# Kernel optimization log

Hardware: AMD Instinct MI355X
Metric: run time of the kernel (lower is better)

The kernel has to match this reference:

```python
import jax, jax.numpy as jnp
import numpy as np

NEG_SLOPE = 0.2  # PyG GATConv default negative_slope
EPS = 1e-16


def gat_conv(x, W, att_src, att_dst, bias, src, dst, heads, out_ch, concat):
    """PyG-style GATConv (eval mode, self-loops already included in src/dst).
    x: [N, F_in]; W: [heads*out_ch, F_in]; att_src/att_dst: [1, heads, out_ch]; bias: [heads*out_ch] or [out_ch].
    """
    N = x.shape[0]
    h = (x @ W.T).reshape(N, heads, out_ch)            # [N, H, C]
    a_src = (h * att_src).sum(-1)                      # [N, H]
    a_dst = (h * att_dst).sum(-1)                      # [N, H]
    alpha = jax.nn.leaky_relu(a_src[src] + a_dst[dst], NEG_SLOPE)  # [E, H]
    # segment softmax over destination nodes
    amax = jax.ops.segment_max(alpha, dst, num_segments=N)         # [N, H]
    ex = jnp.exp(alpha - amax[dst])
    denom = jax.ops.segment_sum(ex, dst, num_segments=N)           # [N, H]
    coef = ex / (denom[dst] + EPS)                                 # [E, H]
    out = jax.ops.segment_sum(h[src] * coef[:, :, None], dst, num_segments=N)  # [N, H, C]
    if concat:
        out = out.reshape(N, heads * out_ch)
    else:
        out = out.mean(axis=1)
    return out + bias


def setup_inputs() -> dict:
    key = jax.random.key(0)
    ks = jax.random.split(key, 10)
    N, F_in, H, C, OUT, E = 50000, 128, 4, 64, 2, 800000
    x = jax.random.normal(ks[0], (N, F_in), dtype=jnp.float32)
    edge_index = jax.random.randint(ks[1], (2, E), 0, N, dtype=jnp.int64)
    glorot = lambda k, shp: jax.random.normal(k, shp, dtype=jnp.float32) * jnp.sqrt(2.0 / (shp[0] + shp[-1]))
    W1 = glorot(ks[2], (H * C, F_in))
    att_src1 = glorot(ks[3], (1, H, C))
    att_dst1 = glorot(ks[4], (1, H, C))
    b1 = jnp.zeros((H * C,), dtype=jnp.float32)
    W2 = glorot(ks[5], (1 * OUT, H * C))
    att_src2 = glorot(ks[6], (1, 1, OUT))
    att_dst2 = glorot(ks[7], (1, 1, OUT))
    b2 = jnp.zeros((OUT,), dtype=jnp.float32)
    return {"x": x, "edge_index": edge_index, "W1": W1, "att_src1": att_src1,
            "att_dst1": att_dst1, "b1": b1, "W2": W2, "att_src2": att_src2,
            "att_dst2": att_dst2, "b2": b2}


def reference(x, edge_index, W1, att_src1, att_dst1, b1, W2, att_src2, att_dst2, b2):
    N = x.shape[0]
    loop = jnp.arange(N, dtype=edge_index.dtype)
    src = jnp.concatenate([edge_index[0], loop])   # add self-loops (PyG default)
    dst = jnp.concatenate([edge_index[1], loop])
    h = gat_conv(x, W1, att_src1, att_dst1, b1, src, dst, heads=4, out_ch=64, concat=True)
    h = jax.nn.relu(h)
    out = gat_conv(h, W2, att_src2, att_dst2, b2, src, dst, heads=1, out_ch=2, concat=False)
    return out
```

## Files before the change

### kernel.cpp

```cpp
#include <hip/hip_runtime.h>
#include <hip/hip_bf16.h>
#include <stdint.h>
#include <math.h>

#define NEG_SLOPE 0.2f
#define EPSV 1e-16f
#define SLOT 64
#define NBQ 128
#define NBUCKET 391
#define CAPA 32
#define EPB 8192
#define OVCAP 64
#define NW1C 16

#define KA 0.8656170245333781f
#define KB 0.5770780163555854f

typedef __attribute__((ext_vector_type(8))) short bf16x8;
typedef __attribute__((ext_vector_type(4))) float f32x4;

static __device__ __forceinline__ float b2f(unsigned short u) {
    union { float f; uint32_t i; } v; v.i = ((uint32_t)u) << 16; return v.f;
}
static __device__ __forceinline__ uint32_t qpk(float a, float b) {
    union { float f; uint32_t u; } x, y; x.f = a; y.f = b;
    return ((x.u + 0x8000u) >> 16) | ((y.u + 0x8000u) & 0xFFFF0000u);
}

__global__ __launch_bounds__(256) void prep_bin_kernel(
    const int* __restrict__ ei, int E,
    const float* __restrict__ W1,
    const float* __restrict__ b1, const float* __restrict__ W2,
    unsigned int* __restrict__ bins, unsigned short* __restrict__ counts,
    unsigned int* __restrict__ gov, unsigned int* __restrict__ govcnt,
    unsigned short* __restrict__ w1p,
    float* __restrict__ b1p, float* __restrict__ w2p0, float* __restrict__ w2p1,
    unsigned short* __restrict__ h1, float4* __restrict__ a_src1v,
    float4* __restrict__ h2pk,
    int N, int nblk_binA)
{
    const int b = blockIdx.x, t = threadIdx.x;

    if (b < nblk_binA) {
        __shared__ unsigned int binS[NBUCKET * CAPA];
        __shared__ unsigned int binC[NBUCKET];
        __shared__ unsigned int ovn;
        const int blk = b;

        for (int i = t; i < NBUCKET; i += 256) binC[i] = 0;
        if (t == 0) ovn = 0;
        __syncthreads();

        const int e_base = blk * EPB;
        for (int i = 0; i < EPB / 256; ++i) {
            int e = e_base + i * 256 + t;
            if (e < E) {
                int s = ei[e], d = ei[E + e];
                int bk = d >> 7;
                unsigned int w = (unsigned int)s | ((unsigned int)(d & 127) << 16)
                               | ((unsigned int)bk << 23);
                unsigned int r = atomicAdd(&binC[bk], 1u);
                if (r < CAPA) binS[bk * CAPA + r] = w;
                else {
                    unsigned int o = atomicAdd(&ovn, 1u);
                    if (o < OVCAP) gov[blk * OVCAP + o] = w;
                }
            }
        }
        __syncthreads();

        for (int wdx = t; wdx < NBUCKET * CAPA; wdx += 256) {
            int bk = wdx >> 5, sl = wdx & 31;
            bins[((size_t)bk * nblk_binA + blk) * CAPA + sl] = binS[wdx];
        }
        for (int i = t; i < NBUCKET; i += 256) {
            unsigned int c = binC[i];
            counts[(size_t)i * nblk_binA + blk] = (unsigned short)(c < CAPA ? c : CAPA);
        }
        if (t == 0) govcnt[blk] = (ovn < OVCAP ? ovn : OVCAP);
    } else if (b < nblk_binA + NW1C) {
        int idx = (b - nblk_binA) * 256 + t;
        int c = idx >> 4, oct = idx & 15;
        int ct = c >> 4, l15 = c & 15;
        int kk = oct >> 2, quad = oct & 3;
        const float* sp = W1 + (size_t)c * 128 + oct * 8;
        float4 u0 = *(const float4*)(sp);
        float4 u1 = *(const float4*)(sp + 4);
        uint4 w;
        w.x = qpk(u0.x, u0.y); w.y = qpk(u0.z, u0.w);
        w.z = qpk(u1.x, u1.y); w.w = qpk(u1.z, u1.w);
        *(uint4*)(w1p + (size_t)(((kk * 16 + ct) * 4 + quad) * 128 + l15 * 8)) = w;
    } else {
        int cp = t;
        int c = (cp & 15) * 16 + (cp >> 4);
        b1p[cp]  = b1[c];
        w2p0[cp] = W2[c];
        w2p1[cp] = W2[256 + c];
        if (t < 32)
            ((uint4*)(h1 + (size_t)N * 256))[t] = make_uint4(0, 0, 0, 0);
        else if (t == 32)
            a_src1v[N] = make_float4(-1e4f, -1e4f, -1e4f, -1e4f);
        else if (t == 33)
            h2pk[N] = make_float4(0.f, 0.f, -1e4f, 0.f);
    }
}

__global__ __launch_bounds__(256, 3) void gemm_front_kernel(
    const float* __restrict__ x,
    const unsigned short* __restrict__ w1p,
    const float* __restrict__ att_src1, const float* __restrict__ att_dst1,
    unsigned short* __restrict__ h1,
    float4* __restrict__ a_src1v, float4* __restrict__ a_dst1v,
    int N)
{
    const int t = threadIdx.x;
    const int wv = t >> 6, lane = t & 63;
    const int l15 = lane & 15, quad = lane >> 4;
    const int m0 = blockIdx.x * 64 + wv * 16;

    union { bf16x8 v; uint32_t u[4]; } A[4];
    {
        int m = m0 + l15;
        int mr = m < N ? m : N - 1;
        const float* ap = x + (size_t)mr * 128 + quad * 8;
        #pragma unroll
        for (int kk = 0; kk < 4; ++kk) {
            float4 u0 = *(const float4*)(ap + kk * 32);
            float4 u1 = *(const float4*)(ap + kk * 32 + 4);
            A[kk].u[0] = qpk(u0.x, u0.y);
            A[kk].u[1] = qpk(u0.z, u0.w);
            A[kk].u[2] = qpk(u1.x, u1.y);
            A[kk].u[3] = qpk(u1.z, u1.w);
        }
    }

    f32x4 acc[16];
    #pragma unroll
    for (int ct = 0; ct < 16; ++ct) acc[ct] = (f32x4){0.f, 0.f, 0.f, 0.f};

    const size_t bbase = (size_t)quad * 128 + l15 * 8;
    #pragma unroll
    for (int kk = 0; kk < 4; ++kk) {
        #pragma unroll
        for (int ct = 0; ct < 16; ++ct) {
            bf16x8 Bv = *(const bf16x8*)(w1p + (size_t)(kk * 16 + ct) * 512 + bbase);
            acc[ct] = __builtin_amdgcn_mfma_f32_16x16x32_bf16(A[kk].v, Bv, acc[ct], 0, 0, 0);
        }
    }

    #pragma unroll
    for (int r = 0; r < 4; ++r) {
        int m = m0 + quad * 4 + r;
        if (m < N) {
            uint32_t u[8];
            #pragma unroll
            for (int j = 0; j < 8; ++j)
                u[j] = qpk(acc[2 * j][r], acc[2 * j + 1][r]);
            uint4* hp = (uint4*)(h1 + (size_t)m * 256 + l15 * 16);
            hp[0] = make_uint4(u[0], u[1], u[2], u[3]);
            hp[1] = make_uint4(u[4], u[5], u[6], u[7]);
        }
    }

    float as_l[16], ad_l[16];
    #pragma unroll
    for (int ct = 0; ct < 16; ++ct) {
        as_l[ct] = att_src1[ct * 16 + l15];
        ad_l[ct] = att_dst1[ct * 16 + l15];
    }
    #pragma unroll
    for (int r = 0; r < 4; ++r) {
        float ps[4] = {0.f, 0.f, 0.f, 0.f};
        float pd[4] = {0.f, 0.f, 0.f, 0.f};
        #pragma unroll
        for (int ct = 0; ct < 16; ++ct) {
            ps[ct >> 2] += acc[ct][r] * as_l[ct];
            pd[ct >> 2] += acc[ct][r] * ad_l[ct];
        }
        #pragma unroll
        for (int off = 1; off < 16; off <<= 1) {
            #pragma unroll
            for (int hh = 0; hh < 4; ++hh) {
                ps[hh] += __shfl_xor(ps[hh], off);
                pd[hh] += __shfl_xor(pd[hh], off);
            }
        }
        int m = m0 + quad * 4 + r;
        if (l15 == 0 && m < N) {
            a_src1v[m] = make_float4(ps[0], ps[1], ps[2], ps[3]);
            a_dst1v[m] = make_float4(pd[0], pd[1], pd[2], pd[3]);
        }
    }
}

__global__ __launch_bounds__(256) void csr_build_kernel(
    const unsigned int* __restrict__ bins, const unsigned short* __restrict__ counts,
    const unsigned int* __restrict__ gov, const unsigned int* __restrict__ govcnt,
    int* __restrict__ deg, unsigned short* __restrict__ csr16,
    int N, int nblk_binA)
{
    const int b = blockIdx.x, t = threadIdx.x;
    const int base = b * NBQ;
    __shared__ unsigned short lcsr[NBQ * SLOT];
    __shared__ unsigned int ldeg[NBQ];

    const unsigned int pad2 = ((unsigned int)N << 16) | (unsigned int)N;
    unsigned int* lc32 = (unsigned int*)lcsr;
    for (int i = t; i < NBQ * SLOT / 2; i += 256) lc32[i] = pad2;
    __syncthreads();
    for (int i = t; i < NBQ; i += 256) {
        ldeg[i] = 1;
        lcsr[i << 6] = (unsigned short)(base + i);
    }
    __syncthreads();

    if (t < 2 * nblk_binA) {
        int cell = t >> 1;
        int c = counts[(size_t)b * nblk_binA + cell];
        const unsigned int* cp = bins + ((size_t)b * nblk_binA + cell) * CAPA;
        for (int r = (t & 1); r < c; r += 2) {
            unsigned int w = cp[r];
            int dl = (w >> 16) & 127;
            unsigned int rank = atomicAdd(&ldeg[dl], 1u);
            if (rank < SLOT) lcsr[(dl << 6) + rank] = (unsigned short)(w & 0xFFFF);
        }
    }
    for (int idx = t; idx < nblk_binA * OVCAP; idx += 256) {
        int blk = idx >> 6, sl = idx & (OVCAP - 1);
        if (sl < (int)govcnt[blk]) {
            unsigned int w = gov[idx];
            if ((int)(w >> 23) == b) {
                int dl = (w >> 16) & 127;
                unsigned int rank = atomicAdd(&ldeg[dl], 1u);
                if (rank < SLOT) lcsr[(dl << 6) + rank] = (unsigned short)(w & 0xFFFF);
            }
        }
    }
    __syncthreads();

    const int nn = min(NBQ, N - base);
    uint4* dst = (uint4*)(csr16 + (size_t)base * SLOT);
    const uint4* src = (const uint4*)lcsr;
    for (int i = t; i < nn * 8; i += 256) dst[i] = src[i];
    for (int i = t; i < nn; i += 256) deg[base + i] = (int)ldeg[i];
}

__global__ __launch_bounds__(256) void agg1_layer2_kernel(
    const int* __restrict__ deg, const unsigned short* __restrict__ csr16,
    const float* __restrict__ a_src1, const float* __restrict__ a_dst1,
    const unsigned short* __restrict__ h1,
    const float* __restrict__ b1p,
    const float* __restrict__ w2p0, const float* __restrict__ w2p1,
    const float* __restrict__ as2, const float* __restrict__ ad2,
    float4* __restrict__ h2pk, int N)
{
    const int wv = threadIdx.x >> 6, lane = threadIdx.x & 63;
    const int half = lane >> 5, ll = lane & 31;
    const int n = blockIdx.x * 4 + wv;
    if (n >= N) return;
    const int h0 = (ll & 1) * 2;
    const unsigned short* cs = csr16 + (size_t)n * SLOT;
    const int dn = min(deg[n], 57);
    const float2 adh = *(const float2*)(a_dst1 + (size_t)n * 4 + h0);

    const int iters  = (dn + 1) >> 1;
    const int iters4 = (iters + 3) & ~3;

    const unsigned llo = (unsigned)ll * 16u;
    const unsigned ho  = (unsigned)h0 * 4u;
    const char* h1b = (const char*)h1;
    const char* asb = (const char*)a_src1;

    float acc[8] = {0.f, 0.f, 0.f, 0.f, 0.f, 0.f, 0.f, 0.f};
    float den0 = 0.f, den1 = 0.f;

    auto consume = [&](float2 av, uint4 r) {
        float a0 = av.x + adh.x, a1 = av.y + adh.y;
        float e0 = exp2f(fmaf(KB, fabsf(a0), KA * a0));
        float e1 = exp2f(fmaf(KB, fabsf(a1), KA * a1));
        den0 += e0; den1 += e1;
        union { unsigned u; float f; } lo, hi;
        lo.u = r.x << 16; hi.u = r.x & 0xFFFF0000u;
        acc[0] = fmaf(e0, lo.f, acc[0]); acc[1] = fmaf(e0, hi.f, acc[1]);
        lo.u = r.y << 16; hi.u = r.y & 0xFFFF0000u;
        acc[2] = fmaf(e0, lo.f, acc[2]); acc[3] = fmaf(e0, hi.f, acc[3]);
        lo.u = r.z << 16; hi.u = r.z & 0xFFFF0000u;
        acc[4] = fmaf(e1, lo.f, acc[4]); acc[5] = fmaf(e1, hi.f, acc[5]);
        lo.u = r.w << 16; hi.u = r.w & 0xFFFF0000u;
        acc[6] = fmaf(e1, lo.f, acc[6]); acc[7] = fmaf(e1, hi.f, acc[7]);
    };

    int ia = half, ib = half + 2, ic = half + 4, id = half + 6;
    unsigned s0 = cs[ia], s1 = cs[ib], s2 = cs[ic], s3 = cs[id];
    uint4  rA = *(const uint4*)(h1b + s0 * 512u + llo);
    float2 aA = *(const float2*)(asb + s0 * 16u + ho);
    uint4  rB = *(const uint4*)(h1b + s1 * 512u + llo);
    float2 aB = *(const float2*)(asb + s1 * 16u + ho);
    uint4  rC = *(const uint4*)(h1b + s2 * 512u + llo);
    float2 aC = *(const float2*)(asb + s2 * 16u + ho);
    uint4  rD = *(const uint4*)(h1b + s3 * 512u + llo);
    float2 aD = *(const float2*)(asb + s3 * 16u + ho);

    for (int k = 0; k + 4 < iters4; k += 4) {
        unsigned n0 = cs[ia + 8], n1 = cs[ib + 8], n2 = cs[ic + 8], n3 = cs[id + 8];
        consume(aA, rA);
        rA = *(const uint4*)(h1b + n0 * 512u + llo);
        aA = *(const float2*)(asb + n0 * 16u + ho);
        consume(aB, rB);
        rB = *(const uint4*)(h1b + n1 * 512u + llo);
        aB = *(const float2*)(asb + n1 * 16u + ho);
        consume(aC, rC);
        rC = *(const uint4*)(h1b + n2 * 512u + llo);
        aC = *(const float2*)(asb + n2 * 16u + ho);
        consume(aD, rD);
        rD = *(const uint4*)(h1b + n3 * 512u + llo);
        aD = *(const float2*)(asb + n3 * 16u + ho);
        ia += 8; ib += 8; ic += 8; id += 8;
    }
    consume(aA, rA); consume(aB, rB); consume(aC, rC); consume(aD, rD);

    #pragma unroll
    for (int k = 0; k < 8; ++k) acc[k] += __shfl_xor(acc[k], 32);
    den0 += __shfl_xor(den0, 32);
    den1 += __shfl_xor(den1, 32);

    const float inv0 = 1.f / (den0 + EPSV);
    const float inv1 = 1.f / (den1 + EPSV);
    const int c0 = ll * 8;
    float4 ba = *(const float4*)(b1p + c0);
    float4 bb = *(const float4*)(b1p + c0 + 4);
    float v[8];
    v[0] = acc[0] * inv0 + ba.x; v[1] = acc[1] * inv0 + ba.y;
    v[2] = acc[2] * inv0 + ba.z; v[3] = acc[3] * inv0 + ba.w;
    v[4] = acc[4] * inv1 + bb.x; v[5] = acc[5] * inv1 + bb.y;
    v[6] = acc[6] * inv1 + bb.z; v[7] = acc[7] * inv1 + bb.w;
    #pragma unroll
    for (int k = 0; k < 8; ++k) v[k] = v[k] > 0.f ? v[k] : 0.f;

    float4 w0a = *(const float4*)(w2p0 + c0);
    float4 w0b = *(const float4*)(w2p0 + c0 + 4);
    float4 w1a = *(const float4*)(w2p1 + c0);
    float4 w1b = *(const float4*)(w2p1 + c0 + 4);
    float p0 = v[0]*w0a.x + v[1]*w0a.y + v[2]*w0a.z + v[3]*w0a.w
             + v[4]*w0b.x + v[5]*w0b.y + v[6]*w0b.z + v[7]*w0b.w;
    float p1 = v[0]*w1a.x + v[1]*w1a.y + v[2]*w1a.z + v[3]*w1a.w
             + v[4]*w1b.x + v[5]*w1b.y + v[6]*w1b.z + v[7]*w1b.w;
    #pragma unroll
    for (int off = 16; off; off >>= 1) {
        p0 += __shfl_xor(p0, off);
        p1 += __shfl_xor(p1, off);
    }
    if (lane == 0) {
        h2pk[n] = make_float4(p0, p1,
                              p0 * as2[0] + p1 * as2[1],
                              p0 * ad2[0] + p1 * ad2[1]);
    }
}

__global__ __launch_bounds__(256) void aggregate2_csr_kernel(
    const int* __restrict__ deg, const unsigned short* __restrict__ csr16,
    const float4* __restrict__ h2pk,
    const float* __restrict__ b2, float* __restrict__ out, int N)
{
    const int wv = threadIdx.x >> 6, lane = threadIdx.x & 63;
    const int g = lane >> 4, q = lane & 15;
    const int n = blockIdx.x * 16 + wv * 4 + g;
    if (n >= N) return;
    const unsigned short* cs = csr16 + (size_t)n * SLOT;
    const int dn = min(deg[n], SLOT);
    float ad = h2pk[n].w;
    float den = 0.f, num0 = 0.f, num1 = 0.f;
    const char* hb = (const char*)h2pk;
    const int trip = (dn + 15) >> 4;
    for (int k = 0; k < trip; ++k) {
        unsigned s = cs[q + (k << 4)];
        float4 hq = *(const float4*)(hb + s * 16u);
        float aa = hq.z + ad;
        float ex = exp2f(fmaf(KB, fabsf(aa), KA * aa));
        den += ex;
        num0 = fmaf(ex, hq.x, num0);
        num1 = fmaf(ex, hq.y, num1);
    }
    #pragma unroll
    for (int off = 8; off; off >>= 1) {
        den  += __shfl_xor(den, off);
        num0 += __shfl_xor(num0, off);
        num1 += __shfl_xor(num1, off);
    }
    if (q == 0) {
        float inv = 1.f / (den + EPSV);
        out[(size_t)n * 2]     = num0 * inv + b2[0];
        out[(size_t)n * 2 + 1] = num1 * inv + b2[1];
    }
}

extern "C" void kernel_launch(void* const* d_in, const int* in_sizes, int n_in,
                              void* d_out, int out_size, void* d_ws, size_t ws_size,
                              hipStream_t stream)
{
    const float* x   = (const float*)d_in[0];
    const int*   ei  = (const int*)d_in[1];
    const float* W1  = (const float*)d_in[2];
    const float* as1 = (const float*)d_in[3];
    const float* ad1 = (const float*)d_in[4];
    const float* b1  = (const float*)d_in[5];
    const float* W2  = (const float*)d_in[6];
    const float* as2 = (const float*)d_in[7];
    const float* ad2 = (const float*)d_in[8];
    const float* b2p = (const float*)d_in[9];

    const int N  = in_sizes[0] / 128;
    const int E  = in_sizes[1] / 2;

    const int NB        = (N + NBQ - 1) / NBQ;
    const int nblk_binA = (E + EPB - 1) / EPB;

    char* ws = (char*)d_ws;
    size_t off = 0;
    auto alloc = [&](size_t bytes) -> char* {
        char* p = ws + off;
        off = (off + bytes + 255) & ~(size_t)255;
        return p;
    };
    unsigned short* h1 = (unsigned short*)alloc((size_t)(N + 1) * 256 * 2);
    float* a_src1  = (float*)alloc((size_t)(N + 1) * 4 * 4);
    float* a_dst1  = (float*)alloc((size_t)N * 4 * 4);
    float4* h2pk   = (float4*)alloc((size_t)(N + 1) * 16);
    float* b1pp    = (float*)alloc((size_t)256 * 4);
    float* w2p0    = (float*)alloc((size_t)256 * 4);
    float* w2p1    = (float*)alloc((size_t)256 * 4);
    int*   deg     = (int*)alloc((size_t)N * 4);
    unsigned short* csr16 = (unsigned short*)alloc((size_t)N * SLOT * 2);
    unsigned int*   bins  = (unsigned int*)alloc((size_t)NB * nblk_binA * CAPA * 4);
    unsigned short* cnts  = (unsigned short*)alloc((size_t)NB * nblk_binA * 2);
    unsigned int*   gov   = (unsigned int*)alloc((size_t)nblk_binA * OVCAP * 4);
    unsigned int*   govcnt= (unsigned int*)alloc((size_t)nblk_binA * 4);
    unsigned short* w1pb  = (unsigned short*)alloc((size_t)256 * 128 * 2);

    prep_bin_kernel<<<nblk_binA + NW1C + 1, 256, 0, stream>>>(
        ei, E, W1, b1, W2,
        bins, cnts, gov, govcnt, w1pb, b1pp, w2p0, w2p1,
        h1, (float4*)a_src1, h2pk, N, nblk_binA);
    gemm_front_kernel<<<(N + 63) / 64, 256, 0, stream>>>(
        x, w1pb, as1, ad1, h1, (float4*)a_src1, (float4*)a_dst1, N);
    csr_build_kernel<<<NB, 256, 0, stream>>>(
        bins, cnts, gov, govcnt, deg, csr16, N, nblk_binA);
    agg1_layer2_kernel<<<(N + 3) / 4, 256, 0, stream>>>(
        deg, csr16, a_src1, a_dst1, h1,
        b1pp, w2p0, w2p1, as2, ad2, h2pk, N);
    aggregate2_csr_kernel<<<(N + 15) / 16, 256, 0, stream>>>(
        deg, csr16, h2pk, b2p, (float*)d_out, N);
}
```

Measured before the change: 201.0 us.

## Merge GEMM and CSR build into one launch; trim padded aggregation iterations

Combines the layer-1 GEMM kernel and the CSR build kernel into a single launch whose blocks branch by block index, so the two independent stages can run concurrently and one kernel launch is saved. The aggregation kernel no longer rounds its loop count up to a multiple of four; it consumes only the prefetched edges that remain, which skips wasted padded gathers. The merged kernel makes GEMM blocks carry the 16KB shared buffer used only by CSR blocks and shares a launch-bound setting across both paths, which may lower occupancy for the GEMM part.

```diff
diff --git a/kernel.cpp b/kernel.cpp
--- a/kernel.cpp
+++ b/kernel.cpp
@@ -105,144 +105,143 @@
     }
 }
 
-__global__ __launch_bounds__(256, 3) void gemm_front_kernel(
+__global__ __launch_bounds__(256, 3) void gemm_csr_kernel(
     const float* __restrict__ x,
     const unsigned short* __restrict__ w1p,
     const float* __restrict__ att_src1, const float* __restrict__ att_dst1,
     unsigned short* __restrict__ h1,
     float4* __restrict__ a_src1v, float4* __restrict__ a_dst1v,
-    int N)
-{
-    const int t = threadIdx.x;
-    const int wv = t >> 6, lane = t & 63;
-    const int l15 = lane & 15, quad = lane >> 4;
-    const int m0 = blockIdx.x * 64 + wv * 16;
-
-    union { bf16x8 v; uint32_t u[4]; } A[4];
-    {
-        int m = m0 + l15;
-        int mr = m < N ? m : N - 1;
-        const float* ap = x + (size_t)mr * 128 + quad * 8;
-        #pragma unroll
-        for (int kk = 0; kk < 4; ++kk) {
-            float4 u0 = *(const float4*)(ap + kk * 32);
-            float4 u1 = *(const float4*)(ap + kk * 32 + 4);
-            A[kk].u[0] = qpk(u0.x, u0.y);
-            A[kk].u[1] = qpk(u0.z, u0.w);
-            A[kk].u[2] = qpk(u1.x, u1.y);
-            A[kk].u[3] = qpk(u1.z, u1.w);
-        }
-    }
-
-    f32x4 acc[16];
-    #pragma unroll
-    for (int ct = 0; ct < 16; ++ct) acc[ct] = (f32x4){0.f, 0.f, 0.f, 0.f};
-
-    const size_t bbase = (size_t)quad * 128 + l15 * 8;
-    #pragma unroll
-    for (int kk = 0; kk < 4; ++kk) {
-        #pragma unroll
-        for (int ct = 0; ct < 16; ++ct) {
-            bf16x8 Bv = *(const bf16x8*)(w1p + (size_t)(kk * 16 + ct) * 512 + bbase);
-            acc[ct] = __builtin_amdgcn_mfma_f32_16x16x32_bf16(A[kk].v, Bv, acc[ct], 0, 0, 0);
-        }
-    }
-
-    #pragma unroll
-    for (int r = 0; r < 4; ++r) {
-        int m = m0 + quad * 4 + r;
-        if (m < N) {
-            uint32_t u[8];
-            #pragma unroll
-            for (int j = 0; j < 8; ++j)
-                u[j] = qpk(acc[2 * j][r], acc[2 * j + 1][r]);
-            uint4* hp = (uint4*)(h1 + (size_t)m * 256 + l15 * 16);
-            hp[0] = make_uint4(u[0], u[1], u[2], u[3]);
-            hp[1] = make_uint4(u[4], u[5], u[6], u[7]);
-        }
-    }
-
-    float as_l[16], ad_l[16];
-    #pragma unroll
-    for (int ct = 0; ct < 16; ++ct) {
-        as_l[ct] = att_src1[ct * 16 + l15];
-        ad_l[ct] = att_dst1[ct * 16 + l15];
-    }
-    #pragma unroll
-    for (int r = 0; r < 4; ++r) {
-        float ps[4] = {0.f, 0.f, 0.f, 0.f};
-        float pd[4] = {0.f, 0.f, 0.f, 0.f};
-        #pragma unroll
-        for (int ct = 0; ct < 16; ++ct) {
-            ps[ct >> 2] += acc[ct][r] * as_l[ct];
-            pd[ct >> 2] += acc[ct][r] * ad_l[ct];
-        }
-        #pragma unroll
-        for (int off = 1; off < 16; off <<= 1) {
-            #pragma unroll
-            for (int hh = 0; hh < 4; ++hh) {
-                ps[hh] += __shfl_xor(ps[hh], off);
-                pd[hh] += __shfl_xor(pd[hh], off);
-            }
-        }
-        int m = m0 + quad * 4 + r;
-        if (l15 == 0 && m < N) {
-            a_src1v[m] = make_float4(ps[0], ps[1], ps[2], ps[3]);
-            a_dst1v[m] = make_float4(pd[0], pd[1], pd[2], pd[3]);
-        }
-    }
-}
-
-__global__ __launch_bounds__(256) void csr_build_kernel(
     const unsigned int* __restrict__ bins, const unsigned short* __restrict__ counts,
     const unsigned int* __restrict__ gov, const unsigned int* __restrict__ govcnt,
     int* __restrict__ deg, unsigned short* __restrict__ csr16,
-    int N, int nblk_binA)
+    int N, int nblk_gemm, int nblk_binA)
 {
-    const int b = blockIdx.x, t = threadIdx.x;
-    const int base = b * NBQ;
+    const int t = threadIdx.x;
     __shared__ unsigned short lcsr[NBQ * SLOT];
     __shared__ unsigned int ldeg[NBQ];
 
-    const unsigned int pad2 = ((unsigned int)N << 16) | (unsigned int)N;
-    unsigned int* lc32 = (unsigned int*)lcsr;
-    for (int i = t; i < NBQ * SLOT / 2; i += 256) lc32[i] = pad2;
-    __syncthreads();
-    for (int i = t; i < NBQ; i += 256) {
-        ldeg[i] = 1;
-        lcsr[i << 6] = (unsigned short)(base + i);
-    }
-    __syncthreads();
-
-    if (t < 2 * nblk_binA) {
-        int cell = t >> 1;
-        int c = counts[(size_t)b * nblk_binA + cell];
-        const unsigned int* cp = bins + ((size_t)b * nblk_binA + cell) * CAPA;
-        for (int r = (t & 1); r < c; r += 2) {
-            unsigned int w = cp[r];
-            int dl = (w >> 16) & 127;
-            unsigned int rank = atomicAdd(&ldeg[dl], 1u);
-            if (rank < SLOT) lcsr[(dl << 6) + rank] = (unsigned short)(w & 0xFFFF);
-        }
-    }
-    for (int idx = t; idx < nblk_binA * OVCAP; idx += 256) {
-        int blk = idx >> 6, sl = idx & (OVCAP - 1);
-        if (sl < (int)govcnt[blk]) {
-            unsigned int w = gov[idx];
-            if ((int)(w >> 23) == b) {
+    if (blockIdx.x < nblk_gemm) {
+        const int wv = t >> 6, lane = t & 63;
+        const int l15 = lane & 15, quad = lane >> 4;
+        const int m0 = blockIdx.x * 64 + wv * 16;
+
+        union { bf16x8 v; uint32_t u[4]; } A[4];
+        {
+            int m = m0 + l15;
+            int mr = m < N ? m : N - 1;
+            const float* ap = x + (size_t)mr * 128 + quad * 8;
+            #pragma unroll
+            for (int kk = 0; kk < 4; ++kk) {
+                float4 u0 = *(const float4*)(ap + kk * 32);
+                float4 u1 = *(const float4*)(ap + kk * 32 + 4);
+                A[kk].u[0] = qpk(u0.x, u0.y);
+                A[kk].u[1] = qpk(u0.z, u0.w);
+                A[kk].u[2] = qpk(u1.x, u1.y);
+                A[kk].u[3] = qpk(u1.z, u1.w);
+            }
+        }
+
+        f32x4 acc[16];
+        #pragma unroll
+        for (int ct = 0; ct < 16; ++ct) acc[ct] = (f32x4){0.f, 0.f, 0.f, 0.f};
+
+        const size_t bbase = (size_t)quad * 128 + l15 * 8;
+        #pragma unroll
+        for (int kk = 0; kk < 4; ++kk) {
+            #pragma unroll
+            for (int ct = 0; ct < 16; ++ct) {
+                bf16x8 Bv = *(const bf16x8*)(w1p + (size_t)(kk * 16 + ct) * 512 + bbase);
+                acc[ct] = __builtin_amdgcn_mfma_f32_16x16x32_bf16(A[kk].v, Bv, acc[ct], 0, 0, 0);
+            }
+        }
+
+        #pragma unroll
+        for (int r = 0; r < 4; ++r) {
+            int m = m0 + quad * 4 + r;
+            if (m < N) {
+                uint32_t u[8];
+                #pragma unroll
+                for (int j = 0; j < 8; ++j)
+                    u[j] = qpk(acc[2 * j][r], acc[2 * j + 1][r]);
+                uint4* hp = (uint4*)(h1 + (size_t)m * 256 + l15 * 16);
+                hp[0] = make_uint4(u[0], u[1], u[2], u[3]);
+                hp[1] = make_uint4(u[4], u[5], u[6], u[7]);
+            }
+        }
+
+        float as_l[16], ad_l[16];
+        #pragma unroll
+        for (int ct = 0; ct < 16; ++ct) {
+            as_l[ct] = att_src1[ct * 16 + l15];
+            ad_l[ct] = att_dst1[ct * 16 + l15];
+        }
+        #pragma unroll
+        for (int r = 0; r < 4; ++r) {
+            float ps[4] = {0.f, 0.f, 0.f, 0.f};
+            float pd[4] = {0.f, 0.f, 0.f, 0.f};
+            #pragma unroll
+            for (int ct = 0; ct < 16; ++ct) {
+                ps[ct >> 2] += acc[ct][r] * as_l[ct];
+                pd[ct >> 2] += acc[ct][r] * ad_l[ct];
+            }
+            #pragma unroll
+            for (int off = 1; off < 16; off <<= 1) {
+                #pragma unroll
+                for (int hh = 0; hh < 4; ++hh) {
+                    ps[hh] += __shfl_xor(ps[hh], off);
+                    pd[hh] += __shfl_xor(pd[hh], off);
+                }
+            }
+            int m = m0 + quad * 4 + r;
+            if (l15 == 0 && m < N) {
+                a_src1v[m] = make_float4(ps[0], ps[1], ps[2], ps[3]);
+                a_dst1v[m] = make_float4(pd[0], pd[1], pd[2], pd[3]);
+            }
+        }
+    } else {
+        const int b = blockIdx.x - nblk_gemm;
+        const int base = b * NBQ;
+
+        const unsigned int pad2 = ((unsigned int)N << 16) | (unsigned int)N;
+        unsigned int* lc32 = (unsigned int*)lcsr;
+        for (int i = t; i < NBQ * SLOT / 2; i += 256) lc32[i] = pad2;
+        __syncthreads();
+        for (int i = t; i < NBQ; i += 256) {
+            ldeg[i] = 1;
+            lcsr[i << 6] = (unsigned short)(base + i);
+        }
+        __syncthreads();
+
+        if (t < 2 * nblk_binA) {
+            int cell = t >> 1;
+            int c = counts[(size_t)b * nblk_binA + cell];
+            const unsigned int* cp = bins + ((size_t)b * nblk_binA + cell) * CAPA;
+            for (int r = (t & 1); r < c; r += 2) {
+                unsigned int w = cp[r];
                 int dl = (w >> 16) & 127;
                 unsigned int rank = atomicAdd(&ldeg[dl], 1u);
                 if (rank < SLOT) lcsr[(dl << 6) + rank] = (unsigned short)(w & 0xFFFF);
             }
         }
-    }
-    __syncthreads();
-
-    const int nn = min(NBQ, N - base);
-    uint4* dst = (uint4*)(csr16 + (size_t)base * SLOT);
-    const uint4* src = (const uint4*)lcsr;
-    for (int i = t; i < nn * 8; i += 256) dst[i] = src[i];
-    for (int i = t; i < nn; i += 256) deg[base + i] = (int)ldeg[i];
+        for (int idx = t; idx < nblk_binA * OVCAP; idx += 256) {
+            int blk = idx >> 6, sl = idx & (OVCAP - 1);
+            if (sl < (int)govcnt[blk]) {
+                unsigned int w = gov[idx];
+                if ((int)(w >> 23) == b) {
+                    int dl = (w >> 16) & 127;
+                    unsigned int rank = atomicAdd(&ldeg[dl], 1u);
+                    if (rank < SLOT) lcsr[(dl << 6) + rank] = (unsigned short)(w & 0xFFFF);
+                }
+            }
+        }
+        __syncthreads();
+
+        const int nn = min(NBQ, N - base);
+        uint4* dst = (uint4*)(csr16 + (size_t)base * SLOT);
+        const uint4* src = (const uint4*)lcsr;
+        for (int i = t; i < nn * 8; i += 256) dst[i] = src[i];
+        for (int i = t; i < nn; i += 256) deg[base + i] = (int)ldeg[i];
+    }
 }
 
 __global__ __launch_bounds__(256) void agg1_layer2_kernel(
@@ -263,8 +262,7 @@
     const int dn = min(deg[n], 57);
     const float2 adh = *(const float2*)(a_dst1 + (size_t)n * 4 + h0);
 
-    const int iters  = (dn + 1) >> 1;
-    const int iters4 = (iters + 3) & ~3;
+    const int iters = (dn + 1) >> 1;
 
     const unsigned llo = (unsigned)ll * 16u;
     const unsigned ho  = (unsigned)h0 * 4u;
@@ -301,7 +299,8 @@
     uint4  rD = *(const uint4*)(h1b + s3 * 512u + llo);
     float2 aD = *(const float2*)(asb + s3 * 16u + ho);
 
-    for (int k = 0; k + 4 < iters4; k += 4) {
+    int k = 0;
+    for (; k + 4 < iters; k += 4) {
         unsigned n0 = cs[ia + 8], n1 = cs[ib + 8], n2 = cs[ic + 8], n3 = cs[id + 8];
         consume(aA, rA);
         rA = *(const uint4*)(h1b + n0 * 512u + llo);
@@ -317,10 +316,14 @@
         aD = *(const float2*)(asb + n3 * 16u + ho);
         ia += 8; ib += 8; ic += 8; id += 8;
     }
-    consume(aA, rA); consume(aB, rB); consume(aC, rC); consume(aD, rD);
+    const int rem = iters - k;
+    consume(aA, rA);
+    if (rem > 1) consume(aB, rB);
+    if (rem > 2) consume(aC, rC);
+    if (rem > 3) consume(aD, rD);
 
     #pragma unroll
-    for (int k = 0; k < 8; ++k) acc[k] += __shfl_xor(acc[k], 32);
+    for (int kq = 0; kq < 8; ++kq) acc[kq] += __shfl_xor(acc[kq], 32);
     den0 += __shfl_xor(den0, 32);
     den1 += __shfl_xor(den1, 32);
 
@@ -335,7 +338,7 @@
     v[4] = acc[4] * inv1 + bb.x; v[5] = acc[5] * inv1 + bb.y;
     v[6] = acc[6] * inv1 + bb.z; v[7] = acc[7] * inv1 + bb.w;
     #pragma unroll
-    for (int k = 0; k < 8; ++k) v[k] = v[k] > 0.f ? v[k] : 0.f;
+    for (int kq = 0; kq < 8; ++kq) v[kq] = v[kq] > 0.f ? v[kq] : 0.f;
 
     float4 w0a = *(const float4*)(w2p0 + c0);
     float4 w0b = *(const float4*)(w2p0 + c0 + 4);
@@ -413,6 +416,7 @@
     const int E  = in_sizes[1] / 2;
 
     const int NB        = (N + NBQ - 1) / NBQ;
+    const int nblk_gemm = (N + 63) / 64;
     const int nblk_binA = (E + EPB - 1) / EPB;
 
     char* ws = (char*)d_ws;
@@ -441,10 +445,9 @@
         ei, E, W1, b1, W2,
         bins, cnts, gov, govcnt, w1pb, b1pp, w2p0, w2p1,
         h1, (float4*)a_src1, h2pk, N, nblk_binA);
-    gemm_front_kernel<<<(N + 63) / 64, 256, 0, stream>>>(
-        x, w1pb, as1, ad1, h1, (float4*)a_src1, (float4*)a_dst1, N);
-    csr_build_kernel<<<NB, 256, 0, stream>>>(
-        bins, cnts, gov, govcnt, deg, csr16, N, nblk_binA);
+    gemm_csr_kernel<<<nblk_gemm + NB, 256, 0, stream>>>(
+        x, w1pb, as1, ad1, h1, (float4*)a_src1, (float4*)a_dst1,
+        bins, cnts, gov, govcnt, deg, csr16, N, nblk_gemm, nblk_binA);
     agg1_layer2_kernel<<<(N + 3) / 4, 256, 0, stream>>>(
         deg, csr16, a_src1, a_dst1, h1,
         b1pp, w2p0, w2p1, as2, ad2, h2pk, N);
```

Result: faster. 193.9 us (-3.5%).
